# Kernel optimization log

Hardware: AMD Instinct MI355X
Metric: run time of the kernel (lower is better)

The kernel has to match this reference:

```python
import jax, jax.numpy as jnp
import numpy as np

EPS = 1e-6

def _ln(x):
    # LayerNorm without affine, eps=1e-6
    mu = jnp.mean(x, axis=-1, keepdims=True)
    var = jnp.var(x, axis=-1, keepdims=True)
    return (x - mu) * jax.lax.rsqrt(var + EPS)

def setup_inputs() -> dict:
    key = jax.random.key(0)
    ks = jax.random.split(key, 12)
    B, N, C = 8, 1024, 768
    H = 12
    Hf = 4 * C  # mlp hidden
    s = 0.02
    return {
        "x": jax.random.normal(ks[0], (B, N, C), jnp.float32),
        "c": jax.random.normal(ks[1], (B, C), jnp.float32),
        "qkv_w": jax.random.normal(ks[2], (3 * C, C), jnp.float32) * s,
        "qkv_b": jax.random.normal(ks[3], (3 * C,), jnp.float32) * s,
        "proj_w": jax.random.normal(ks[4], (C, C), jnp.float32) * s,
        "proj_b": jax.random.normal(ks[5], (C,), jnp.float32) * s,
        "fc1_w": jax.random.normal(ks[6], (Hf, C), jnp.float32) * s,
        "fc1_b": jax.random.normal(ks[7], (Hf,), jnp.float32) * s,
        "fc2_w": jax.random.normal(ks[8], (C, Hf), jnp.float32) * s,
        "fc2_b": jax.random.normal(ks[9], (C,), jnp.float32) * s,
        "ada_w": jax.random.normal(ks[10], (6 * C, C), jnp.float32) * s,
        "ada_b": jax.random.normal(ks[11], (6 * C,), jnp.float32) * s,
    }

def reference(x, c, qkv_w, qkv_b, proj_w, proj_b, fc1_w, fc1_b, fc2_w, fc2_b, ada_w, ada_b):
    B, N, C = x.shape
    H = 12
    D = C // H
    scale = D ** -0.5

    # adaLN_modulation: SiLU then Linear -> chunk into 6 [B, C] pieces
    ada = jax.nn.silu(c) @ ada_w.T + ada_b  # [B, 6C]
    sh_msa, sc_msa, g_msa, sh_mlp, sc_mlp, g_mlp = jnp.split(ada, 6, axis=1)

    def modulate(h, shift, scale_):
        return h * (1 + scale_[:, None, :]) + shift[:, None, :]

    # --- attention branch ---
    h = modulate(_ln(x), sh_msa, sc_msa)
    qkv = h @ qkv_w.T + qkv_b                       # [B, N, 3C]
    qkv = qkv.reshape(B, N, 3, H, D)
    q, k, v = qkv[:, :, 0], qkv[:, :, 1], qkv[:, :, 2]   # [B, N, H, D]
    attn = jnp.einsum('bnhd,bmhd->bhnm', q, k) * scale   # [B, H, N, N]
    attn = jax.nn.softmax(attn, axis=-1)
    o = jnp.einsum('bhnm,bmhd->bnhd', attn, v).reshape(B, N, C)
    o = o @ proj_w.T + proj_b
    x = x + g_msa[:, None, :] * o

    # --- MLP branch ---
    h = modulate(_ln(x), sh_mlp, sc_mlp)
    h = jax.nn.gelu(h @ fc1_w.T + fc1_b, approximate=False)
    h = h @ fc2_w.T + fc2_b
    x = x + g_mlp[:, None, :] * h
    return x
```

## Files before the change

kernel.cpp:

```cpp
#include <hip/hip_runtime.h>
#include <hip/hip_bf16.h>
#include <math.h>

typedef __attribute__((ext_vector_type(8))) short bf16x8;
typedef __attribute__((ext_vector_type(4))) float f32x4;

__device__ __forceinline__ unsigned short f2bf(float f) {
  union { float f; unsigned int u; } v; v.f = f;
  unsigned int u = v.u;
  u += 0x7fffu + ((u >> 16) & 1u);
  return (unsigned short)(u >> 16);
}

__device__ __forceinline__ void gl2l16(const unsigned short* g, unsigned short* l) {
  __builtin_amdgcn_global_load_lds(
      (const __attribute__((address_space(1))) unsigned int*)g,
      (__attribute__((address_space(3))) unsigned int*)l, 16, 0, 0);
}

__global__ __launch_bounds__(256) void k_f2bf4(const float4* __restrict__ src,
                                               ushort4* __restrict__ dst, int n4) {
  int i = blockIdx.x * 256 + threadIdx.x;
  if (i < n4) {
    float4 f = src[i];
    ushort4 o;
    o.x = f2bf(f.x); o.y = f2bf(f.y); o.z = f2bf(f.z); o.w = f2bf(f.w);
    dst[i] = o;
  }
}

__global__ __launch_bounds__(256) void k_ada(const float* __restrict__ c,
                                             const float* __restrict__ ada_w,
                                             const float* __restrict__ ada_b,
                                             float* __restrict__ ada) {
  __shared__ float sc[8 * 768];
  __shared__ float red[4][64][8];
  const int t = threadIdx.x;
  for (int i = t; i < 8 * 768; i += 256) {
    float v = c[i];
    sc[i] = v / (1.f + __expf(-v));
  }
  __syncthreads();
  const int cl = t & 63, ks = t >> 6;
  const int col = blockIdx.x * 64 + cl;
  float acc[8];
#pragma unroll
  for (int b = 0; b < 8; b++) acc[b] = 0.f;
  const float* wr = ada_w + (size_t)col * 768 + ks * 192;
  for (int k = 0; k < 192; k += 4) {
    float4 w = *(const float4*)&wr[k];
    const int kk = ks * 192 + k;
#pragma unroll
    for (int b = 0; b < 8; b++) {
      acc[b] += sc[b * 768 + kk] * w.x + sc[b * 768 + kk + 1] * w.y +
                sc[b * 768 + kk + 2] * w.z + sc[b * 768 + kk + 3] * w.w;
    }
  }
#pragma unroll
  for (int b = 0; b < 8; b++) red[ks][cl][b] = acc[b];
  __syncthreads();
  if (ks == 0) {
    const float bj = ada_b[col];
#pragma unroll
    for (int b = 0; b < 8; b++)
      ada[b * 4608 + col] = red[0][cl][b] + red[1][cl][b] + red[2][cl][b] + red[3][cl][b] + bj;
  }
}

__global__ __launch_bounds__(256) void k_ln_mod(const float* __restrict__ x,
                                                const float* __restrict__ ada,
                                                int sh_off, int sc_off,
                                                unsigned short* __restrict__ h) {
  const int row = blockIdx.x, t = threadIdx.x, b = row >> 10;
  const float* xr = x + (size_t)row * 768;
  float v0 = xr[t], v1 = xr[t + 256], v2 = xr[t + 512];
  float s = v0 + v1 + v2;
  float ss = v0 * v0 + v1 * v1 + v2 * v2;
#pragma unroll
  for (int m = 1; m < 64; m <<= 1) {
    s += __shfl_xor(s, m);
    ss += __shfl_xor(ss, m);
  }
  __shared__ float red[8];
  if ((t & 63) == 0) { red[t >> 6] = s; red[4 + (t >> 6)] = ss; }
  __syncthreads();
  const float S = red[0] + red[1] + red[2] + red[3];
  const float SS = red[4] + red[5] + red[6] + red[7];
  const float mean = S * (1.f / 768.f);
  const float var = SS * (1.f / 768.f) - mean * mean;
  const float inv = rsqrtf(var + 1e-6f);
  const float* sh = ada + b * 4608 + sh_off;
  const float* scp = ada + b * 4608 + sc_off;
  unsigned short* hr = h + (size_t)row * 768;
  float vv[3] = {v0, v1, v2};
#pragma unroll
  for (int i = 0; i < 3; i++) {
    int cx = t + i * 256;
    float hh = (vv[i] - mean) * inv;
    hh = hh * (1.f + scp[cx]) + sh[cx];
    hr[cx] = f2bf(hh);
  }
}

template <int EPI, int TN>
__global__ __launch_bounds__(256) void k_gemm(const unsigned short* __restrict__ A,
                                              const unsigned short* __restrict__ B,
                                              const float* __restrict__ bias,
                                              int M, int N, int K,
                                              const float* __restrict__ resid,
                                              const float* __restrict__ ada, int goff,
                                              float* __restrict__ outf,
                                              unsigned short* __restrict__ outb,
                                              unsigned short* __restrict__ vt) {
  constexpr int MI = (TN == 128) ? 4 : 2;
  __shared__ __align__(16) unsigned short Asm[128 * 32];
  __shared__ __align__(16) unsigned short Bsm[TN * 32];
  const int t = threadIdx.x;
  const int w = t >> 6, lane = t & 63, l = lane & 15, qd = lane >> 4;
  const int bn = blockIdx.x * TN, bm = blockIdx.y * 128;
  const int wm = (TN == 128) ? (w >> 1) * 64 : w * 32;
  const int wn = (TN == 128) ? (w & 1) * 64 : 0;

  const int srow = t >> 2;
  const int scol = ((t & 3) ^ ((srow >> 1) & 3)) * 8;
  const unsigned short* Ap0 = A + (size_t)(bm + srow) * K + scol;
  const unsigned short* Ap1 = A + (size_t)(bm + 64 + srow) * K + scol;
  const unsigned short* Bp0 = B + (size_t)(bn + srow) * K + scol;
  const unsigned short* Bp1 = B + (size_t)(bn + 64 + srow) * K + scol;
  unsigned short* Adst0 = &Asm[w * 512];
  unsigned short* Adst1 = &Asm[2048 + w * 512];
  unsigned short* Bdst0 = &Bsm[w * 512];
  unsigned short* Bdst1 = &Bsm[(TN == 128 ? 2048 : 0) + w * 512];

  f32x4 acc[MI][4];
#pragma unroll
  for (int i = 0; i < MI; i++)
#pragma unroll
    for (int j = 0; j < 4; j++) acc[i][j] = {0.f, 0.f, 0.f, 0.f};

  const int swz = (l >> 1) & 3;

  for (int k0 = 0; k0 < K; k0 += 32) {
    gl2l16(Ap0 + k0, Adst0);
    gl2l16(Ap1 + k0, Adst1);
    gl2l16(Bp0 + k0, Bdst0);
    if (TN == 128) gl2l16(Bp1 + k0, Bdst1);
    __syncthreads();
    bf16x8 af[MI], bfr[4];
#pragma unroll
    for (int i = 0; i < MI; i++)
      af[i] = *(const bf16x8*)&Asm[(wm + i * 16 + l) * 32 + ((qd ^ swz) << 3)];
#pragma unroll
    for (int j = 0; j < 4; j++)
      bfr[j] = *(const bf16x8*)&Bsm[(wn + j * 16 + l) * 32 + ((qd ^ swz) << 3)];
#pragma unroll
    for (int i = 0; i < MI; i++)
#pragma unroll
      for (int j = 0; j < 4; j++)
        acc[i][j] = __builtin_amdgcn_mfma_f32_16x16x32_bf16(af[i], bfr[j], acc[i][j], 0, 0, 0);
    __syncthreads();
  }

#pragma unroll
  for (int i = 0; i < MI; i++) {
#pragma unroll
    for (int j = 0; j < 4; j++) {
      const int gn = bn + wn + j * 16 + l;
      const float bv = bias[gn];
#pragma unroll
      for (int r = 0; r < 4; r++) {
        const int gm = bm + wm + i * 16 + qd * 4 + r;
        float v = acc[i][j][r] + bv;
        if (EPI == 0) {
          if (gn < 1536) {
            outb[(size_t)gm * 1536 + gn] = f2bf(v);
          } else {
            const int hh = (gn - 1536) >> 6, dd = (gn - 1536) & 63;
            const int bb = gm >> 10, nn = gm & 1023;
            vt[(((size_t)bb * 12 + hh) * 64 + dd) * 1024 + nn] = f2bf(v);
          }
        } else if (EPI == 2) {
          float ge = 0.5f * v * (1.f + erff(v * 0.70710678118f));
          outb[(size_t)gm * N + gn] = f2bf(ge);
        } else {
          const int bb = gm >> 10;
          const float g = ada[bb * 4608 + goff + gn];
          outf[(size_t)gm * 768 + gn] = resid[(size_t)gm * 768 + gn] + g * v;
        }
      }
    }
  }
}

__global__ __launch_bounds__(256) void k_attn(const unsigned short* __restrict__ qk,
                                              const unsigned short* __restrict__ vt,
                                              unsigned short* __restrict__ o) {
  __shared__ __align__(16) unsigned short Ksm[64 * 76];
  __shared__ __align__(16) unsigned short Vsm[64 * 76];
  __shared__ __align__(16) unsigned short Psm[128 * 76];
  const int t = threadIdx.x;
  const int qb = blockIdx.x, h = blockIdx.y, b = blockIdx.z;
  const int w = t >> 6, lane = t & 63, l = lane & 15, qd = lane >> 4;

  const size_t qrow0 = (size_t)(b * 1024 + qb * 128 + w * 32 + l);
  bf16x8 qf[2][2];
#pragma unroll
  for (int mt = 0; mt < 2; mt++)
#pragma unroll
    for (int ks = 0; ks < 2; ks++)
      qf[mt][ks] = *(const bf16x8*)&qk[(qrow0 + mt * 16) * 1536 + h * 64 + ks * 32 + qd * 8];

  f32x4 oacc[2][4];
  float rsum[2][4];
#pragma unroll
  for (int mt = 0; mt < 2; mt++)
#pragma unroll
    for (int j = 0; j < 4; j++) { oacc[mt][j] = {0.f, 0.f, 0.f, 0.f}; rsum[mt][j] = 0.f; }

  const size_t kbase = (size_t)b * 1024 * 1536 + 768 + h * 64;
  const size_t vbase = ((size_t)(b * 12 + h)) * 64 * 1024;

  for (int k0 = 0; k0 < 1024; k0 += 64) {
    for (int idx = t; idx < 512; idx += 256) {
      const int row = idx >> 3, ch = (idx & 7) * 8;
      *(bf16x8*)&Ksm[row * 76 + ch] =
          *(const bf16x8*)&qk[kbase + (size_t)(k0 + row) * 1536 + ch];
      *(bf16x8*)&Vsm[row * 76 + ch] =
          *(const bf16x8*)&vt[vbase + (size_t)row * 1024 + k0 + ch];
    }
    __syncthreads();

    bf16x8 kf[4][2];
#pragma unroll
    for (int ct = 0; ct < 4; ct++)
#pragma unroll
      for (int ks = 0; ks < 2; ks++)
        kf[ct][ks] = *(const bf16x8*)&Ksm[(ct * 16 + l) * 76 + ks * 32 + qd * 8];

#pragma unroll
    for (int mt = 0; mt < 2; mt++) {
      f32x4 s[4];
#pragma unroll
      for (int ct = 0; ct < 4; ct++) {
        f32x4 a = {0.f, 0.f, 0.f, 0.f};
        a = __builtin_amdgcn_mfma_f32_16x16x32_bf16(qf[mt][0], kf[ct][0], a, 0, 0, 0);
        a = __builtin_amdgcn_mfma_f32_16x16x32_bf16(qf[mt][1], kf[ct][1], a, 0, 0, 0);
        s[ct] = a;
      }
#pragma unroll
      for (int ct = 0; ct < 4; ct++) {
#pragma unroll
        for (int r = 0; r < 4; r++) {
          float p = __expf(s[ct][r] * 0.125f);
          rsum[mt][r] += p;
          Psm[(w * 32 + mt * 16 + qd * 4 + r) * 76 + ct * 16 + l] = f2bf(p);
        }
      }
    }

    bf16x8 vf[4][2];
#pragma unroll
    for (int dt = 0; dt < 4; dt++)
#pragma unroll
      for (int ks = 0; ks < 2; ks++)
        vf[dt][ks] = *(const bf16x8*)&Vsm[(dt * 16 + l) * 76 + ks * 32 + qd * 8];
#pragma unroll
    for (int mt = 0; mt < 2; mt++) {
      bf16x8 pf0 = *(const bf16x8*)&Psm[(w * 32 + mt * 16 + l) * 76 + qd * 8];
      bf16x8 pf1 = *(const bf16x8*)&Psm[(w * 32 + mt * 16 + l) * 76 + 32 + qd * 8];
#pragma unroll
      for (int dt = 0; dt < 4; dt++) {
        oacc[mt][dt] = __builtin_amdgcn_mfma_f32_16x16x32_bf16(pf0, vf[dt][0], oacc[mt][dt], 0, 0, 0);
        oacc[mt][dt] = __builtin_amdgcn_mfma_f32_16x16x32_bf16(pf1, vf[dt][1], oacc[mt][dt], 0, 0, 0);
      }
    }
    __syncthreads();
  }

#pragma unroll
  for (int mt = 0; mt < 2; mt++)
#pragma unroll
    for (int r = 0; r < 4; r++) {
      float rs = rsum[mt][r];
#pragma unroll
      for (int mk = 1; mk < 16; mk <<= 1) rs += __shfl_xor(rs, mk);
      const float inv = 1.f / rs;
      const size_t orow = (size_t)(b * 1024 + qb * 128 + w * 32 + mt * 16 + qd * 4 + r);
#pragma unroll
      for (int dt = 0; dt < 4; dt++)
        o[orow * 768 + h * 64 + dt * 16 + l] = f2bf(oacc[mt][dt][r] * inv);
    }
}

extern "C" void kernel_launch(void* const* d_in, const int* in_sizes, int n_in,
                              void* d_out, int out_size, void* d_ws, size_t ws_size,
                              hipStream_t stream) {
  const float* x      = (const float*)d_in[0];
  const float* c      = (const float*)d_in[1];
  const float* qkv_w  = (const float*)d_in[2];
  const float* qkv_b  = (const float*)d_in[3];
  const float* proj_w = (const float*)d_in[4];
  const float* proj_b = (const float*)d_in[5];
  const float* fc1_w  = (const float*)d_in[6];
  const float* fc1_b  = (const float*)d_in[7];
  const float* fc2_w  = (const float*)d_in[8];
  const float* fc2_b  = (const float*)d_in[9];
  const float* ada_w  = (const float*)d_in[10];
  const float* ada_b  = (const float*)d_in[11];
  float* out = (float*)d_out;

  char* ws = (char*)d_ws;
  float*          ada       = (float*)(ws + 0);
  unsigned short* qkv_w_bf  = (unsigned short*)(ws + 147456);
  unsigned short* proj_w_bf = (unsigned short*)(ws + 3686400);
  unsigned short* fc1_w_bf  = (unsigned short*)(ws + 4866048);
  unsigned short* fc2_w_bf  = (unsigned short*)(ws + 9584640);
  unsigned short* h_bf      = (unsigned short*)(ws + 14303232);
  unsigned short* qk_bf     = (unsigned short*)(ws + 26886144);
  unsigned short* vt_bf     = (unsigned short*)(ws + 52051968);
  unsigned short* o_bf      = (unsigned short*)(ws + 64634880);
  float*          x1        = (float*)(ws + 77217792);
  unsigned short* f1_bf     = qk_bf;

  k_f2bf4<<<1728, 256, 0, stream>>>((const float4*)qkv_w, (ushort4*)qkv_w_bf, 442368);
  k_f2bf4<<<576, 256, 0, stream>>>((const float4*)proj_w, (ushort4*)proj_w_bf, 147456);
  k_f2bf4<<<2304, 256, 0, stream>>>((const float4*)fc1_w, (ushort4*)fc1_w_bf, 589824);
  k_f2bf4<<<2304, 256, 0, stream>>>((const float4*)fc2_w, (ushort4*)fc2_w_bf, 589824);

  k_ada<<<72, 256, 0, stream>>>(c, ada_w, ada_b, ada);

  k_ln_mod<<<8192, 256, 0, stream>>>(x, ada, 0, 768, h_bf);

  k_gemm<0, 128><<<dim3(18, 64), 256, 0, stream>>>(h_bf, qkv_w_bf, qkv_b, 8192, 2304, 768,
                                                   nullptr, nullptr, 0, nullptr, qk_bf, vt_bf);

  k_attn<<<dim3(8, 12, 8), 256, 0, stream>>>(qk_bf, vt_bf, o_bf);

  k_gemm<1, 64><<<dim3(12, 64), 256, 0, stream>>>(o_bf, proj_w_bf, proj_b, 8192, 768, 768,
                                                  x, ada, 1536, x1, nullptr, nullptr);

  k_ln_mod<<<8192, 256, 0, stream>>>(x1, ada, 2304, 3072, h_bf);

  k_gemm<2, 128><<<dim3(24, 64), 256, 0, stream>>>(h_bf, fc1_w_bf, fc1_b, 8192, 3072, 768,
                                                   nullptr, nullptr, 0, nullptr, f1_bf, nullptr);

  k_gemm<3, 64><<<dim3(12, 64), 256, 0, stream>>>(f1_bf, fc2_w_bf, fc2_b, 8192, 768, 3072,
                                                  x1, ada, 3840, out, nullptr, nullptr);
}
```

Before: 456.3 us.

## Widen GEMM K-step to 64, remap blocks per XCD, merge weight conversions

The GEMM now loads two 32-wide K slices per iteration into two LDS buffers, which halves the number of barrier pairs per tile. A 1D grid is remapped so that consecutive blocks on the same XCD share the same A row-block, improving L2 reuse. The four fp32-to-bf16 weight conversion launches are merged into a single kernel. The cost is doubled LDS per block, which may reduce occupancy, plus some extra index arithmetic.

```diff
diff --git a/kernel.cpp b/kernel.cpp
--- a/kernel.cpp
+++ b/kernel.cpp
@@ -18,15 +18,20 @@
       (__attribute__((address_space(3))) unsigned int*)l, 16, 0, 0);
 }
 
-__global__ __launch_bounds__(256) void k_f2bf4(const float4* __restrict__ src,
-                                               ushort4* __restrict__ dst, int n4) {
+__global__ __launch_bounds__(256) void k_conv(const float4* __restrict__ s0, ushort4* __restrict__ d0,
+                                              const float4* __restrict__ s1, ushort4* __restrict__ d1,
+                                              const float4* __restrict__ s2, ushort4* __restrict__ d2,
+                                              const float4* __restrict__ s3, ushort4* __restrict__ d3) {
   int i = blockIdx.x * 256 + threadIdx.x;
-  if (i < n4) {
-    float4 f = src[i];
-    ushort4 o;
-    o.x = f2bf(f.x); o.y = f2bf(f.y); o.z = f2bf(f.z); o.w = f2bf(f.w);
-    dst[i] = o;
-  }
+  const float4* s; ushort4* d; int off;
+  if (i < 442368) { s = s0; d = d0; off = i; }
+  else if (i < 589824) { s = s1; d = d1; off = i - 442368; }
+  else if (i < 1179648) { s = s2; d = d2; off = i - 589824; }
+  else { s = s3; d = d3; off = i - 1179648; }
+  float4 f = s[off];
+  ushort4 o;
+  o.x = f2bf(f.x); o.y = f2bf(f.y); o.z = f2bf(f.z); o.w = f2bf(f.w);
+  d[off] = o;
 }
 
 __global__ __launch_bounds__(256) void k_ada(const float* __restrict__ c,
@@ -106,18 +111,25 @@
 __global__ __launch_bounds__(256) void k_gemm(const unsigned short* __restrict__ A,
                                               const unsigned short* __restrict__ B,
                                               const float* __restrict__ bias,
-                                              int M, int N, int K,
+                                              int N, int K, int nbx,
                                               const float* __restrict__ resid,
                                               const float* __restrict__ ada, int goff,
                                               float* __restrict__ outf,
                                               unsigned short* __restrict__ outb,
                                               unsigned short* __restrict__ vt) {
   constexpr int MI = (TN == 128) ? 4 : 2;
-  __shared__ __align__(16) unsigned short Asm[128 * 32];
-  __shared__ __align__(16) unsigned short Bsm[TN * 32];
+  __shared__ __align__(16) unsigned short Asm[2][128 * 32];
+  __shared__ __align__(16) unsigned short Bsm[2][TN * 32];
   const int t = threadIdx.x;
   const int w = t >> 6, lane = t & 63, l = lane & 15, qd = lane >> 4;
-  const int bn = blockIdx.x * TN, bm = blockIdx.y * 128;
+
+  const int id = blockIdx.x;
+  const int xcd = id & 7, jj = id >> 3;
+  const int jm = jj / nbx;
+  const int bmi = xcd + (jm << 3);
+  const int bni = jj - jm * nbx;
+  const int bn = bni * TN, bm = bmi * 128;
+
   const int wm = (TN == 128) ? (w >> 1) * 64 : w * 32;
   const int wn = (TN == 128) ? (w & 1) * 64 : 0;
 
@@ -127,10 +139,6 @@
   const unsigned short* Ap1 = A + (size_t)(bm + 64 + srow) * K + scol;
   const unsigned short* Bp0 = B + (size_t)(bn + srow) * K + scol;
   const unsigned short* Bp1 = B + (size_t)(bn + 64 + srow) * K + scol;
-  unsigned short* Adst0 = &Asm[w * 512];
-  unsigned short* Adst1 = &Asm[2048 + w * 512];
-  unsigned short* Bdst0 = &Bsm[w * 512];
-  unsigned short* Bdst1 = &Bsm[(TN == 128 ? 2048 : 0) + w * 512];
 
   f32x4 acc[MI][4];
 #pragma unroll
@@ -140,24 +148,30 @@
 
   const int swz = (l >> 1) & 3;
 
-  for (int k0 = 0; k0 < K; k0 += 32) {
-    gl2l16(Ap0 + k0, Adst0);
-    gl2l16(Ap1 + k0, Adst1);
-    gl2l16(Bp0 + k0, Bdst0);
-    if (TN == 128) gl2l16(Bp1 + k0, Bdst1);
+  for (int k0 = 0; k0 < K; k0 += 64) {
+#pragma unroll
+    for (int s = 0; s < 2; s++) {
+      gl2l16(Ap0 + k0 + 32 * s, &Asm[s][w * 512]);
+      gl2l16(Ap1 + k0 + 32 * s, &Asm[s][2048 + w * 512]);
+      gl2l16(Bp0 + k0 + 32 * s, &Bsm[s][w * 512]);
+      if (TN == 128) gl2l16(Bp1 + k0 + 32 * s, &Bsm[s][2048 + w * 512]);
+    }
     __syncthreads();
-    bf16x8 af[MI], bfr[4];
-#pragma unroll
-    for (int i = 0; i < MI; i++)
-      af[i] = *(const bf16x8*)&Asm[(wm + i * 16 + l) * 32 + ((qd ^ swz) << 3)];
-#pragma unroll
-    for (int j = 0; j < 4; j++)
-      bfr[j] = *(const bf16x8*)&Bsm[(wn + j * 16 + l) * 32 + ((qd ^ swz) << 3)];
-#pragma unroll
-    for (int i = 0; i < MI; i++)
+#pragma unroll
+    for (int s = 0; s < 2; s++) {
+      bf16x8 af[MI], bfr[4];
+#pragma unroll
+      for (int i = 0; i < MI; i++)
+        af[i] = *(const bf16x8*)&Asm[s][(wm + i * 16 + l) * 32 + ((qd ^ swz) << 3)];
 #pragma unroll
       for (int j = 0; j < 4; j++)
-        acc[i][j] = __builtin_amdgcn_mfma_f32_16x16x32_bf16(af[i], bfr[j], acc[i][j], 0, 0, 0);
+        bfr[j] = *(const bf16x8*)&Bsm[s][(wn + j * 16 + l) * 32 + ((qd ^ swz) << 3)];
+#pragma unroll
+      for (int i = 0; i < MI; i++)
+#pragma unroll
+        for (int j = 0; j < 4; j++)
+          acc[i][j] = __builtin_amdgcn_mfma_f32_16x16x32_bf16(af[i], bfr[j], acc[i][j], 0, 0, 0);
+    }
     __syncthreads();
   }
 
@@ -322,28 +336,28 @@
   float*          x1        = (float*)(ws + 77217792);
   unsigned short* f1_bf     = qk_bf;
 
-  k_f2bf4<<<1728, 256, 0, stream>>>((const float4*)qkv_w, (ushort4*)qkv_w_bf, 442368);
-  k_f2bf4<<<576, 256, 0, stream>>>((const float4*)proj_w, (ushort4*)proj_w_bf, 147456);
-  k_f2bf4<<<2304, 256, 0, stream>>>((const float4*)fc1_w, (ushort4*)fc1_w_bf, 589824);
-  k_f2bf4<<<2304, 256, 0, stream>>>((const float4*)fc2_w, (ushort4*)fc2_w_bf, 589824);
+  k_conv<<<6912, 256, 0, stream>>>((const float4*)qkv_w, (ushort4*)qkv_w_bf,
+                                   (const float4*)proj_w, (ushort4*)proj_w_bf,
+                                   (const float4*)fc1_w, (ushort4*)fc1_w_bf,
+                                   (const float4*)fc2_w, (ushort4*)fc2_w_bf);
 
   k_ada<<<72, 256, 0, stream>>>(c, ada_w, ada_b, ada);
 
   k_ln_mod<<<8192, 256, 0, stream>>>(x, ada, 0, 768, h_bf);
 
-  k_gemm<0, 128><<<dim3(18, 64), 256, 0, stream>>>(h_bf, qkv_w_bf, qkv_b, 8192, 2304, 768,
-                                                   nullptr, nullptr, 0, nullptr, qk_bf, vt_bf);
+  k_gemm<0, 128><<<18 * 64, 256, 0, stream>>>(h_bf, qkv_w_bf, qkv_b, 2304, 768, 18,
+                                              nullptr, nullptr, 0, nullptr, qk_bf, vt_bf);
 
   k_attn<<<dim3(8, 12, 8), 256, 0, stream>>>(qk_bf, vt_bf, o_bf);
 
-  k_gemm<1, 64><<<dim3(12, 64), 256, 0, stream>>>(o_bf, proj_w_bf, proj_b, 8192, 768, 768,
-                                                  x, ada, 1536, x1, nullptr, nullptr);
+  k_gemm<1, 64><<<12 * 64, 256, 0, stream>>>(o_bf, proj_w_bf, proj_b, 768, 768, 12,
+                                             x, ada, 1536, x1, nullptr, nullptr);
 
   k_ln_mod<<<8192, 256, 0, stream>>>(x1, ada, 2304, 3072, h_bf);
 
-  k_gemm<2, 128><<<dim3(24, 64), 256, 0, stream>>>(h_bf, fc1_w_bf, fc1_b, 8192, 3072, 768,
-                                                   nullptr, nullptr, 0, nullptr, f1_bf, nullptr);
-
-  k_gemm<3, 64><<<dim3(12, 64), 256, 0, stream>>>(f1_bf, fc2_w_bf, fc2_b, 8192, 768, 3072,
-                                                  x1, ada, 3840, out, nullptr, nullptr);
-}
+  k_gemm<2, 128><<<24 * 64, 256, 0, stream>>>(h_bf, fc1_w_bf, fc1_b, 3072, 768, 24,
+                                              nullptr, nullptr, 0, nullptr, f1_bf, nullptr);
+
+  k_gemm<3, 64><<<12 * 64, 256, 0, stream>>>(f1_bf, fc2_w_bf, fc2_b, 768, 3072, 12,
+                                             x1, ada, 3840, out, nullptr, nullptr);
+}
```

New measurement: 416.5 us. 1.1x faster.
